# Kernel tuning notes

Measured on AMD Instinct MI355X. Metric: run time of the kernel, lower is better.

Reference implementation:

```python
import jax, jax.numpy as jnp
import numpy as np

DIM = 1024
NUM_HEADS = 16
HEAD_DIM = DIM // NUM_HEADS


def setup_inputs() -> dict:
    key = jax.random.key(0)
    ks = jax.random.split(key, 5)
    B, T = 2, 2048
    x = jax.random.normal(ks[0], (B, T, DIM), dtype=jnp.float32)
    s = 1.0 / np.sqrt(DIM)
    W_qkv = jax.random.normal(ks[1], (DIM, 3 * DIM), dtype=jnp.float32) * s
    b_qkv = jnp.zeros((3 * DIM,), dtype=jnp.float32)
    W_out = jax.random.normal(ks[2], (DIM, DIM), dtype=jnp.float32) * s
    b_out = jnp.zeros((DIM,), dtype=jnp.float32)
    return {"x": x, "W_qkv": W_qkv, "b_qkv": b_qkv, "W_out": W_out, "b_out": b_out}


def reference(x, W_qkv, b_qkv, W_out, b_out):
    B, T, D = x.shape
    H, Hd = NUM_HEADS, HEAD_DIM
    qkv = x @ W_qkv + b_qkv                       # [B,T,3D]
    qkv = qkv.reshape(B, T, 3, H, Hd)
    q = jnp.transpose(qkv[:, :, 0], (0, 2, 1, 3))  # [B,H,T,Hd]
    k = jnp.transpose(qkv[:, :, 1], (0, 2, 1, 3))
    v = jnp.transpose(qkv[:, :, 2], (0, 2, 1, 3))
    att = jnp.einsum('bhqd,bhkd->bhqk', q, k) / np.sqrt(Hd)  # [B,H,T,T]
    causal = jnp.tril(jnp.ones((T, T), dtype=bool))
    att = jnp.where(causal[None, None], att, -jnp.inf)
    att = jax.nn.softmax(att, axis=-1)
    out = jnp.einsum('bhqk,bhkd->bhqd', att, v)   # [B,H,T,Hd]
    out = jnp.transpose(out, (0, 2, 1, 3)).reshape(B, T, D)
    return out @ W_out + b_out
```

## Files before the change

### kernel.cpp

```cpp
#include <hip/hip_runtime.h>
#include <hip/hip_bf16.h>

typedef unsigned short u16;
typedef __attribute__((ext_vector_type(8))) short short8;
typedef __attribute__((ext_vector_type(4))) float f32x4;
typedef __attribute__((ext_vector_type(4))) unsigned short u16x4;

#define LOG2E 1.44269504088896340736f


__device__ __forceinline__ void gl_lds16(const void* g, void* l) {
  __builtin_amdgcn_global_load_lds(
      (__attribute__((address_space(1))) void*)g,
      (__attribute__((address_space(3))) void*)l, 16, 0, 0);
}

__device__ __forceinline__ float exp2_fast(float x) {
#if __has_builtin(__builtin_amdgcn_exp2f)
  return __builtin_amdgcn_exp2f(x);
#else
  return exp2f(x);
#endif
}

__device__ __forceinline__ u16 f2bf(float f) {
  union { float f; unsigned int i; } v;
  v.f = f;
  unsigned int r = v.i + 0x7fffu + ((v.i >> 16) & 1u);
  return (u16)(r >> 16);
}

__device__ __forceinline__ unsigned int pack_bf2(float lo, float hi) {
  union { __hip_bfloat162 h2; unsigned int u; } c;
  c.h2 = __float22bfloat162_rn(make_float2(lo, hi));
  return c.u;
}


__global__ __launch_bounds__(256) void prep_kernel(
    const float4* __restrict__ x, u16x4* __restrict__ xb,
    const float* __restrict__ Wqkv, u16* __restrict__ WqkvT,
    const float* __restrict__ Wout, u16* __restrict__ WoutT) {
  __shared__ u16 t[64][65];
  int bid = blockIdx.x, tid = threadIdx.x;
  if (bid < 4096) {
    int i = bid * 256 + tid;
    float4 v = x[i];
    u16x4 o;
    o.x = f2bf(v.x); o.y = f2bf(v.y); o.z = f2bf(v.z); o.w = f2bf(v.w);
    xb[i] = o;
    return;
  }
  const float* W;
  u16* WT;
  int K = 1024, N, bxx, byy;
  if (bid < 4864) {
    int tt = bid - 4096;
    W = Wqkv; WT = WqkvT; N = 3072; bxx = tt % 48; byy = tt / 48;
  } else {
    int tt = bid - 4864;
    W = Wout; WT = WoutT; N = 1024; bxx = tt % 16; byy = tt / 16;
  }
  int r0 = byy * 64, c0 = bxx * 64;
  int tx = tid & 63, ty = tid >> 6;
  for (int r = ty; r < 64; r += 4)
    t[r][tx] = f2bf(W[(size_t)(r0 + r) * N + c0 + tx]);
  __syncthreads();
  for (int r = ty; r < 64; r += 4)
    WT[(size_t)(c0 + r) * K + r0 + tx] = t[tx][r];
}


template <bool OUT_F32, int BN>
__global__ __launch_bounds__(256) void gemm_bt_kernel(
    const u16* __restrict__ A, const u16* __restrict__ Bt,
    const float* __restrict__ bias, void* __restrict__ Cout,
    int M, int N, int K) {
  constexpr int NBJ = BN / 32;
  constexpr int CH_A = 16;
  constexpr int CH_B = BN / 8;
  constexpr int PER_W = (CH_A + CH_B) / 4;
  __shared__ u16 As[128 * 64];
  __shared__ u16 Bs[BN * 64];
  int tid = threadIdx.x;
  int w = tid >> 6, lane = tid & 63, l15 = lane & 15, quad = lane >> 4;
  int m0 = blockIdx.y * 128, n0 = blockIdx.x * BN;
  int wm = (w & 1) * 64, wn = (w >> 1) * (BN / 2);

  f32x4 acc[4][NBJ];
#pragma unroll
  for (int i = 0; i < 4; ++i)
#pragma unroll
    for (int j = 0; j < NBJ; ++j) {
      f32x4 z = {0.f, 0.f, 0.f, 0.f};
      acc[i][j] = z;
    }

  int r8 = lane >> 3;
  int sw = ((lane & 7) ^ r8) * 8;

  for (int kt = 0; kt < K; kt += 64) {
    __syncthreads();
#pragma unroll
    for (int i = 0; i < PER_W; ++i) {
      int c = w * PER_W + i;
      if (c < CH_A) {
        int row = m0 + c * 8 + r8;
        gl_lds16(A + (size_t)row * K + kt + sw, As + c * 512);
      } else {
        int cc = c - CH_A;
        int row = n0 + cc * 8 + r8;
        gl_lds16(Bt + (size_t)row * K + kt + sw, Bs + cc * 512);
      }
    }
    __syncthreads();

#pragma unroll
    for (int kh = 0; kh < 2; ++kh) {
      short8 af[4], bf[NBJ];
#pragma unroll
      for (int i = 0; i < 4; ++i) {
        int R = wm + i * 16 + l15;
        af[i] = *(const short8*)(As + R * 64 +
                                 ((kh * 32 + quad * 8) ^ ((R & 7) * 8)));
      }
#pragma unroll
      for (int j = 0; j < NBJ; ++j) {
        int R = wn + j * 16 + l15;
        bf[j] = *(const short8*)(Bs + R * 64 +
                                 ((kh * 32 + quad * 8) ^ ((R & 7) * 8)));
      }
#pragma unroll
      for (int i = 0; i < 4; ++i)
#pragma unroll
        for (int j = 0; j < NBJ; ++j)
          acc[i][j] = __builtin_amdgcn_mfma_f32_16x16x32_bf16(af[i], bf[j],
                                                              acc[i][j], 0, 0, 0);
    }
  }

  float bv[NBJ];
#pragma unroll
  for (int j = 0; j < NBJ; ++j) bv[j] = bias[n0 + wn + j * 16 + l15];
#pragma unroll
  for (int i = 0; i < 4; ++i)
#pragma unroll
    for (int j = 0; j < NBJ; ++j) {
      int col = n0 + wn + j * 16 + l15;
#pragma unroll
      for (int r = 0; r < 4; ++r) {
        int row = m0 + wm + i * 16 + quad * 4 + r;
        float val = acc[i][j][r] + bv[j];
        if (OUT_F32)
          ((float*)Cout)[(size_t)row * N + col] = val;
        else
          ((u16*)Cout)[(size_t)row * N + col] = f2bf(val);
      }
    }
}


__global__ __launch_bounds__(512, 2) void flash_kernel(
    const u16* __restrict__ qkv, u16* __restrict__ att) {
  __shared__ unsigned int SH[16384];

  int tid = threadIdx.x;
  int w = tid >> 6, half = w >> 2, wq = w & 3;
  int lane = tid & 63, l15 = lane & 15, quad = lane >> 4;
  int bx = blockIdx.x;
  int p = bx >> 5, bh = bx & 31, b = bh >> 4, h = bh & 15;
  const int qs[2] = {15 - p, p};
  const int kmax0 = 2 * qs[0] + 1, kmax1 = 2 * p + 1;
  const int jmax = 16 - p;

  const u16* base = qkv + (size_t)b * 2048 * 3072 + h * 64;
  const u16* kb = base + 1024;
  const u16* vb = base + 2048;

  int ht = tid & 255;
  const int krow = ht >> 3, h7 = ht & 7;

  unsigned int* KsH = SH + half * 2048;
  unsigned int* VtH = SH + 4096 + half * 2048;
  unsigned int* Pw = SH + 8192 + w * 1024;

  uint4 kr0 = *(const uint4*)(kb + (size_t)(half * 64 + krow) * 3072 + h7 * 8);
  uint4 kr1 = *(const uint4*)(kb + (size_t)(half * 64 + krow + 32) * 3072 + h7 * 8);
  uint4 vr0 = *(const uint4*)(vb + (size_t)(half * 64 + 2 * krow) * 3072 + h7 * 8);
  uint4 vr1 = *(const uint4*)(vb + (size_t)(half * 64 + 2 * krow + 1) * 3072 + h7 * 8);

  f32x4 o[2][2][4];
#pragma unroll
  for (int t = 0; t < 2; ++t)
#pragma unroll
    for (int qsub = 0; qsub < 2; ++qsub)
#pragma unroll
      for (int jd = 0; jd < 4; ++jd) {
        f32x4 z = {0.f, 0.f, 0.f, 0.f};
        o[t][qsub][jd] = z;
      }
  float lsum[2][2] = {0.f, 0.f, 0.f, 0.f};

  const int psw = (l15 & 7) << 2;
  const float kscale = 0.125f * LOG2E;

  for (int j = 0; j < jmax; ++j) {
    int kt = 2 * j + half;
    __syncthreads();
    *(uint4*)&KsH[32 * krow + ((4 * h7) ^ ((krow & 7) << 2))] = kr0;
    {
      int r1 = krow + 32;
      *(uint4*)&KsH[32 * r1 + ((4 * h7) ^ ((r1 & 7) << 2))] = kr1;
    }
    {
      const u16* av = (const u16*)&vr0;
      const u16* bvp = (const u16*)&vr1;
#pragma unroll
      for (int jj = 0; jj < 8; ++jj) {
        int d = h7 * 8 + jj;
        VtH[32 * d + (krow ^ ((jj ^ h7) << 2))] =
            (unsigned int)av[jj] | ((unsigned int)bvp[jj] << 16);
      }
    }
    __syncthreads();
    if (j + 1 < jmax) {
      int kn = (kt + 2) * 64;
      kr0 = *(const uint4*)(kb + (size_t)(kn + krow) * 3072 + h7 * 8);
      kr1 = *(const uint4*)(kb + (size_t)(kn + krow + 32) * 3072 + h7 * 8);
      vr0 = *(const uint4*)(vb + (size_t)(kn + 2 * krow) * 3072 + h7 * 8);
      vr1 = *(const uint4*)(vb + (size_t)(kn + 2 * krow + 1) * 3072 + h7 * 8);
    }

#pragma unroll
    for (int t = 0; t < 2; ++t) {
      int km = t ? kmax1 : kmax0;
      if (kt > km) continue;
      bool last = (kt == km);
      if (last && wq < 2) continue;
      bool domask = last || ((kt == km - 1) && wq < 2);
      int qloc = ((last ? (wq - 2) : wq) << 5) + l15;

      const u16* qtb = base + (size_t)(qs[t] * 128 + wq * 32 + l15) * 3072;
      short8 aq00 = *(const short8*)(qtb + quad * 8);
      short8 aq01 = *(const short8*)(qtb + 32 + quad * 8);
      short8 aq10 = *(const short8*)(qtb + 16 * 3072 + quad * 8);
      short8 aq11 = *(const short8*)(qtb + 16 * 3072 + 32 + quad * 8);

      f32x4 s0[4], s1[4];
#pragma unroll
      for (int jn = 0; jn < 4; ++jn) {
        f32x4 z = {0.f, 0.f, 0.f, 0.f};
        s0[jn] = z;
        s1[jn] = z;
      }
#pragma unroll
      for (int ss = 0; ss < 2; ++ss) {
        short8 a0 = ss ? aq01 : aq00;
        short8 a1 = ss ? aq11 : aq10;
#pragma unroll
        for (int jn = 0; jn < 4; ++jn) {
          int row = jn * 16 + l15;
          short8 bk = *(const short8*)&KsH[32 * row + ((16 * ss + 4 * quad) ^
                                                       ((row & 7) << 2))];
          s0[jn] = __builtin_amdgcn_mfma_f32_16x16x32_bf16(bk, a0, s0[jn], 0, 0, 0);
          s1[jn] = __builtin_amdgcn_mfma_f32_16x16x32_bf16(bk, a1, s1[jn], 0, 0, 0);
        }
      }

#pragma unroll
      for (int qsub = 0; qsub < 2; ++qsub) {
        int qq = qloc + qsub * 16;
        float ls = 0.f;
#pragma unroll
        for (int jn = 0; jn < 4; ++jn) {
          f32x4 sv = qsub ? s1[jn] : s0[jn];
          float pv[4];
#pragma unroll
          for (int r = 0; r < 4; ++r) {
            float e = exp2_fast(fmaf(sv[r], kscale, -16.0f));
            if (domask && (jn * 16 + quad * 4 + r > qq)) e = 0.f;
            pv[r] = e;
            ls += e;
          }
          uint2 dd = make_uint2(pack_bf2(pv[0], pv[1]), pack_bf2(pv[2], pv[3]));
          *(uint2*)&Pw[qsub * 512 + 32 * l15 +
                       (((jn << 3) + (quad << 1)) ^ psw)] = dd;
        }
        lsum[t][qsub] += ls;
      }

#pragma unroll
      for (int ss = 0; ss < 2; ++ss) {
        short8 pf0 = *(const short8*)&Pw[32 * l15 +
                                         (((ss << 4) + (quad << 2)) ^ psw)];
        short8 pf1 = *(const short8*)&Pw[512 + 32 * l15 +
                                         (((ss << 4) + (quad << 2)) ^ psw)];
#pragma unroll
        for (int jd = 0; jd < 4; ++jd) {
          int vrow = jd * 16 + l15;
          int f = (vrow & 7) ^ ((vrow >> 3) & 7);
          short8 bvv = *(const short8*)&VtH[32 * vrow +
                                            (((ss << 4) + (quad << 2)) ^ (f << 2))];
          o[t][0][jd] =
              __builtin_amdgcn_mfma_f32_16x16x32_bf16(bvv, pf0, o[t][0][jd], 0, 0, 0);
          o[t][1][jd] =
              __builtin_amdgcn_mfma_f32_16x16x32_bf16(bvv, pf1, o[t][1][jd], 0, 0, 0);
        }
      }
    }
  }

  float lf[2][2];
#pragma unroll
  for (int t = 0; t < 2; ++t)
#pragma unroll
    for (int qsub = 0; qsub < 2; ++qsub) {
      float v = lsum[t][qsub];
      v += __shfl_xor(v, 16, 64);
      v += __shfl_xor(v, 32, 64);
      lf[t][qsub] = v;
    }

  float* OM = (float*)SH;
  float* LM = (float*)(SH + 8704);
  __syncthreads();
#pragma unroll
  for (int t = 0; t < 2; ++t) {
    if (half == 0) {
#pragma unroll
      for (int qsub = 0; qsub < 2; ++qsub) {
        int q = wq * 32 + qsub * 16 + l15;
#pragma unroll
        for (int jd = 0; jd < 4; ++jd)
          *(float4*)&OM[q * 68 + jd * 16 + quad * 4] = *(float4*)&o[t][qsub][jd];
        if (quad == 0) LM[q] = lf[t][qsub];
      }
    }
    __syncthreads();
    if (half == 1) {
#pragma unroll
      for (int qsub = 0; qsub < 2; ++qsub) {
        int q = wq * 32 + qsub * 16 + l15;
        float lr = lf[t][qsub] + LM[q];
        float inv = 1.f / lr;
        size_t row = (size_t)b * 2048 + qs[t] * 128 + q;
        u16* orow = att + row * 1024 + h * 64 + quad * 4;
#pragma unroll
        for (int jd = 0; jd < 4; ++jd) {
          float4 pa = *(float4*)&OM[q * 68 + jd * 16 + quad * 4];
          uint2 dd = make_uint2(pack_bf2((o[t][qsub][jd][0] + pa.x) * inv,
                                         (o[t][qsub][jd][1] + pa.y) * inv),
                                pack_bf2((o[t][qsub][jd][2] + pa.z) * inv,
                                         (o[t][qsub][jd][3] + pa.w) * inv));
          *(uint2*)(orow + jd * 16) = dd;
        }
      }
    }
    __syncthreads();
  }
}


extern "C" void kernel_launch(void* const* d_in, const int* in_sizes, int n_in,
                              void* d_out, int out_size, void* d_ws,
                              size_t ws_size, hipStream_t stream) {
  const float* x = (const float*)d_in[0];
  const float* Wqkv = (const float*)d_in[1];
  const float* bqkv = (const float*)d_in[2];
  const float* Wout = (const float*)d_in[3];
  const float* bout = (const float*)d_in[4];
  float* out = (float*)d_out;

  char* ws = (char*)d_ws;
  u16* WqkvT = (u16*)(ws);
  u16* WoutT = (u16*)(ws + 6291456);
  u16* qkv = (u16*)(ws + 8388608);
  u16* attn = (u16*)(ws + 33554432);
  u16* xb = (u16*)(ws + 41943040);

  prep_kernel<<<5120, 256, 0, stream>>>((const float4*)x, (u16x4*)xb, Wqkv,
                                        WqkvT, Wout, WoutT);
  gemm_bt_kernel<false, 128><<<dim3(24, 32), 256, 0, stream>>>(
      xb, WqkvT, bqkv, (void*)qkv, 4096, 3072, 1024);
  flash_kernel<<<256, 512, 0, stream>>>(qkv, attn);
  gemm_bt_kernel<true, 64><<<dim3(16, 32), 256, 0, stream>>>(
      attn, WoutT, bout, (void*)out, 4096, 1024, 1024);
}
```

Before: 191.7 us.

## Triple-buffer K via direct global-to-LDS loads, double-buffer V, hoist Q fragments

K tiles are now loaded straight into LDS with global_load_lds into a three-slot ring buffer, and V into a two-slot buffer. This lets the loop drop one of its two __syncthreads and replace the other with a single waitcnt plus barrier. Q fragments are loaded once into registers before the loop rather than reloaded from global memory on every iteration. Shared memory grows from 64KB to 112KB per block and register pressure rises from the hoisted Q. Both may lower occupancy under launch_bounds(512,2), and the correctness of the buffer reuse depends on the vmcnt ordering for the async LDS loads.

```diff
diff --git a/kernel.cpp b/kernel.cpp
--- a/kernel.cpp
+++ b/kernel.cpp
@@ -162,7 +162,7 @@
 
 __global__ __launch_bounds__(512, 2) void flash_kernel(
     const u16* __restrict__ qkv, u16* __restrict__ att) {
-  __shared__ unsigned int SH[16384];
+  __shared__ unsigned int SH[28672];
 
   int tid = threadIdx.x;
   int w = tid >> 6, half = w >> 2, wq = w & 3;
@@ -179,13 +179,25 @@
 
   int ht = tid & 255;
   const int krow = ht >> 3, h7 = ht & 7;
-
-  unsigned int* KsH = SH + half * 2048;
-  unsigned int* VtH = SH + 4096 + half * 2048;
-  unsigned int* Pw = SH + 8192 + w * 1024;
-
-  uint4 kr0 = *(const uint4*)(kb + (size_t)(half * 64 + krow) * 3072 + h7 * 8);
-  uint4 kr1 = *(const uint4*)(kb + (size_t)(half * 64 + krow + 32) * 3072 + h7 * 8);
+  const int swk = (h7 ^ (krow & 7)) * 8;
+
+  short8 qf[2][2][2];
+#pragma unroll
+  for (int t = 0; t < 2; ++t) {
+    const u16* qtb = base + (size_t)(qs[t] * 128 + wq * 32 + l15) * 3072;
+    qf[t][0][0] = *(const short8*)(qtb + quad * 8);
+    qf[t][0][1] = *(const short8*)(qtb + 32 + quad * 8);
+    qf[t][1][0] = *(const short8*)(qtb + 16 * 3072 + quad * 8);
+    qf[t][1][1] = *(const short8*)(qtb + 16 * 3072 + 32 + quad * 8);
+  }
+
+  {
+    unsigned int* Ks0 = SH + half * 2048;
+    gl_lds16(kb + (size_t)(half * 64 + krow) * 3072 + swk,
+             (char*)Ks0 + wq * 1024);
+    gl_lds16(kb + (size_t)(half * 64 + 32 + krow) * 3072 + swk,
+             (char*)Ks0 + 4096 + wq * 1024);
+  }
   uint4 vr0 = *(const uint4*)(vb + (size_t)(half * 64 + 2 * krow) * 3072 + h7 * 8);
   uint4 vr1 = *(const uint4*)(vb + (size_t)(half * 64 + 2 * krow + 1) * 3072 + h7 * 8);
 
@@ -203,15 +215,14 @@
 
   const int psw = (l15 & 7) << 2;
   const float kscale = 0.125f * LOG2E;
-
+  unsigned int* Pw = SH + 20480 + w * 1024;
+
+  int b3 = 0;
   for (int j = 0; j < jmax; ++j) {
     int kt = 2 * j + half;
-    __syncthreads();
-    *(uint4*)&KsH[32 * krow + ((4 * h7) ^ ((krow & 7) << 2))] = kr0;
-    {
-      int r1 = krow + 32;
-      *(uint4*)&KsH[32 * r1 + ((4 * h7) ^ ((r1 & 7) << 2))] = kr1;
-    }
+    unsigned int* KsH = SH + b3 * 4096 + half * 2048;
+    unsigned int* VtH = SH + 12288 + (j & 1) * 4096 + half * 2048;
+
     {
       const u16* av = (const u16*)&vr0;
       const u16* bvp = (const u16*)&vr1;
@@ -222,14 +233,23 @@
             (unsigned int)av[jj] | ((unsigned int)bvp[jj] << 16);
       }
     }
-    __syncthreads();
+
+    int nb3 = b3 + 1;
+    if (nb3 == 3) nb3 = 0;
     if (j + 1 < jmax) {
       int kn = (kt + 2) * 64;
-      kr0 = *(const uint4*)(kb + (size_t)(kn + krow) * 3072 + h7 * 8);
-      kr1 = *(const uint4*)(kb + (size_t)(kn + krow + 32) * 3072 + h7 * 8);
+      unsigned int* Ksn = SH + nb3 * 4096 + half * 2048;
+      gl_lds16(kb + (size_t)(kn + krow) * 3072 + swk, (char*)Ksn + wq * 1024);
+      gl_lds16(kb + (size_t)(kn + 32 + krow) * 3072 + swk,
+               (char*)Ksn + 4096 + wq * 1024);
       vr0 = *(const uint4*)(vb + (size_t)(kn + 2 * krow) * 3072 + h7 * 8);
       vr1 = *(const uint4*)(vb + (size_t)(kn + 2 * krow + 1) * 3072 + h7 * 8);
     }
+    b3 = nb3;
+
+    asm volatile("s_waitcnt lgkmcnt(0)" ::: "memory");
+    __builtin_amdgcn_s_barrier();
+    asm volatile("" ::: "memory");
 
 #pragma unroll
     for (int t = 0; t < 2; ++t) {
@@ -240,12 +260,6 @@
       bool domask = last || ((kt == km - 1) && wq < 2);
       int qloc = ((last ? (wq - 2) : wq) << 5) + l15;
 
-      const u16* qtb = base + (size_t)(qs[t] * 128 + wq * 32 + l15) * 3072;
-      short8 aq00 = *(const short8*)(qtb + quad * 8);
-      short8 aq01 = *(const short8*)(qtb + 32 + quad * 8);
-      short8 aq10 = *(const short8*)(qtb + 16 * 3072 + quad * 8);
-      short8 aq11 = *(const short8*)(qtb + 16 * 3072 + 32 + quad * 8);
-
       f32x4 s0[4], s1[4];
 #pragma unroll
       for (int jn = 0; jn < 4; ++jn) {
@@ -255,8 +269,8 @@
       }
 #pragma unroll
       for (int ss = 0; ss < 2; ++ss) {
-        short8 a0 = ss ? aq01 : aq00;
-        short8 a1 = ss ? aq11 : aq10;
+        short8 a0 = qf[t][0][ss];
+        short8 a1 = qf[t][1][ss];
 #pragma unroll
         for (int jn = 0; jn < 4; ++jn) {
           int row = jn * 16 + l15;
```

Result: faster. 169.4 us (-11.6%).
